# Optimization experiments

Measured on AMD Instinct MI355X. Metric: run time of the kernel, lower is better.

Reference implementation:

```python
import jax, jax.numpy as jnp
import numpy as np

N = 20000        # nodes
E = 320000       # edges
F_IN = 512       # feature_size
H = 512          # hidden_dim (z dim)
OUT = 1024       # output_size


def setup_inputs() -> dict:
    key = jax.random.key(0)
    ks = jax.random.split(key, 24)
    p = lambda k, shape: jax.random.normal(k, shape, jnp.float32) * 0.02
    return {
        "x": jax.random.normal(ks[0], (N, F_IN), jnp.float32),
        "edge_index": jax.random.randint(ks[1], (2, E), 0, N),
        "edge_weight": jax.random.uniform(ks[2], (E,), dtype=jnp.float32),
        "beta": jnp.float32(1.0),
        "y_target": jax.random.uniform(ks[3], (1,), dtype=jnp.float32),
        "eps": jax.random.normal(ks[4], (N, H), jnp.float32),
        # GCNConv weights (in_dim, out_dim) + bias
        "W1": p(ks[5], (F_IN, 1024)), "b1": jnp.zeros((1024,), jnp.float32),
        "W2": p(ks[6], (1024, 512)), "b2": jnp.zeros((512,), jnp.float32),
        "W3": p(ks[7], (512, 256)),  "b3": jnp.zeros((256,), jnp.float32),
        # VAE heads
        "Wmu": p(ks[8], (256, H)),  "bmu": jnp.zeros((H,), jnp.float32),
        "Wlv": p(ks[9], (256, H)),  "blv": jnp.zeros((H,), jnp.float32),
        # decoder MLP: (2H+1) -> (2H+1) -> OUT
        "Wd1": p(ks[10], (2 * H + 1, 2 * H + 1)), "bd1": jnp.zeros((2 * H + 1,), jnp.float32),
        "Wd2": p(ks[11], (2 * H + 1, OUT)),       "bd2": jnp.zeros((OUT,), jnp.float32),
    }


def gcn_conv(x, W, b, src, dst, ew):
    # PyG GCNConv: add self-loops (weight 1), symmetric deg normalization,
    # aggregate normalized neighbor messages of x @ W, then add bias.
    xw = x @ W                                             # [N, out]
    deg = jax.ops.segment_sum(ew, dst, num_segments=N) + 1.0
    dinv = jax.lax.rsqrt(deg)                              # [N]
    norm = dinv[src] * ew * dinv[dst]                      # [E]
    agg = jax.ops.segment_sum(norm[:, None] * xw[src], dst, num_segments=N)
    return agg + (dinv * dinv)[:, None] * xw + b


def l2norm(x):
    n = jnp.sqrt(jnp.sum(x * x, axis=1, keepdims=True))
    return x / jnp.maximum(n, 1e-12)


def reference(x, edge_index, edge_weight, beta, y_target, eps,
              W1, b1, W2, b2, W3, b3, Wmu, bmu, Wlv, blv, Wd1, bd1, Wd2, bd2):
    src, dst = edge_index[0], edge_index[1]
    h = jax.nn.relu(l2norm(gcn_conv(x, W1, b1, src, dst, edge_weight)))
    h = jax.nn.relu(l2norm(gcn_conv(h, W2, b2, src, dst, edge_weight)))
    h = jax.nn.relu(l2norm(gcn_conv(h, W3, b3, src, dst, edge_weight)))
    mu = h @ Wmu + bmu                                     # [N, H]
    logvar = h @ Wlv + blv                                 # [N, H]
    # reparameterize(mu, beta * logvar) with eps ~ 0.01 * N(0,1)
    std = jnp.exp(0.5 * beta * logvar)
    z = mu + (0.01 * eps) * std                            # [N, H]
    out1 = jnp.max(z, axis=0, keepdims=True)               # global max pool [1, H]
    out2 = jnp.mean(z, axis=0, keepdims=True)              # global mean pool [1, H]
    reduce_z = jnp.concatenate([out1, out2, y_target[:, None]], axis=-1)  # [1, 2H+1]
    hdec = jax.nn.relu(reduce_z @ Wd1 + bd1)
    recon_x = jax.nn.sigmoid(hdec @ Wd2 + bd2)             # [1, OUT]
    return (recon_x, mu, logvar)
```

## Files before the change

### kernel.cpp

```cpp
#include <hip/hip_runtime.h>

#define NN 20000
#define EE 320000
#define MPAD 20096
#define MTILES 157
#define DKB 128
#define DCH 9

typedef unsigned short u16;
typedef unsigned int u32;
typedef __attribute__((ext_vector_type(8))) short short8;
typedef __attribute__((ext_vector_type(4))) float f32x4;

__device__ inline float bf16lo(u32 u) { return __uint_as_float(u << 16); }
__device__ inline float bf16hi(u32 u) { return __uint_as_float(u & 0xffff0000u); }
__device__ inline u16 f2b(float f) {
  u32 u = __float_as_uint(f);
  u += 0x7fffu + ((u >> 16) & 1u);
  return (u16)(u >> 16);
}
__device__ inline u32 pack2(float a, float b) {
  return (u32)f2b(a) | ((u32)f2b(b) << 16);
}

__device__ inline void gload16(const void* g, void* l) {
  __builtin_amdgcn_global_load_lds(
      (const __attribute__((address_space(1))) void*)g,
      (__attribute__((address_space(3))) void*)l, 16, 0, 0);
}

__device__ inline int xcd_ord(int wg, int nwg) {
  int q = nwg >> 3, r = nwg & 7;
  int xcd = wg & 7, k = wg >> 3;
  return xcd * q + min(xcd, r) + k;
}

__global__ void k_zeroi(int* __restrict__ p, int n) {
  int i = blockIdx.x * blockDim.x + threadIdx.x;
  if (i < n) p[i] = 0;
}

__global__ void k_f2b2(const float* __restrict__ in, u16* __restrict__ out, int npairs) {
  for (int i = blockIdx.x * blockDim.x + threadIdx.x; i < npairs; i += gridDim.x * blockDim.x) {
    float2 v = *(const float2*)(in + 2 * i);
    ((u32*)out)[i] = pack2(v.x, v.y);
  }
}

__global__ void k_wt_all(const float* __restrict__ W1, const float* __restrict__ W2,
                         const float* __restrict__ W3, const float* __restrict__ Wmu,
                         const float* __restrict__ Wlv,
                         u16* __restrict__ T1, u16* __restrict__ T2,
                         u16* __restrict__ T3, u16* __restrict__ Tmu,
                         u16* __restrict__ Tlv) {
  int b = blockIdx.x;
  const float* W; u16* T; int K, N;
  if (b < 2048)      { W = W1;  T = T1;  K = 512;  N = 1024; }
  else if (b < 4096) { W = W2;  T = T2;  K = 1024; N = 512;  b -= 2048; }
  else if (b < 4608) { W = W3;  T = T3;  K = 512;  N = 256;  b -= 4096; }
  else if (b < 5120) { W = Wmu; T = Tmu; K = 256;  N = 512;  b -= 4608; }
  else               { W = Wlv; T = Tlv; K = 256;  N = 512;  b -= 5120; }
  int kb = K >> 8;
  int n = b / kb;
  int k = (b % kb) * 256 + threadIdx.x;
  T[(size_t)n * K + k] = f2b(W[(size_t)k * N + n]);
}

__global__ void k_count(const int* __restrict__ ei, int* __restrict__ counts) {
  int e = blockIdx.x * blockDim.x + threadIdx.x;
  if (e < EE) atomicAdd(counts + ei[EE + e], 1);
}

__global__ __launch_bounds__(256)
void k_scan(const int* __restrict__ counts, int* __restrict__ rowptr, int* __restrict__ cursor) {
  const int CHUNK = (NN + 255) / 256;
  int t = threadIdx.x;
  int lo = t * CHUNK, hi = min(lo + CHUNK, NN);
  int s = 0;
  for (int i = lo; i < hi; ++i) s += counts[i];
  __shared__ int tsum[256];
  tsum[t] = s;
  __syncthreads();
  if (t == 0) {
    int run = 0;
    for (int i = 0; i < 256; ++i) { int v = tsum[i]; tsum[i] = run; run += v; }
  }
  __syncthreads();
  int run = tsum[t];
  for (int i = lo; i < hi; ++i) {
    rowptr[i] = run;
    cursor[i] = run;
    run += counts[i];
  }
  if (t == 255) rowptr[NN] = EE;
}

__global__ void k_fill(const int* __restrict__ ei, const float* __restrict__ ew,
                       int* __restrict__ cursor, int* __restrict__ colsrc,
                       float* __restrict__ ecw) {
  int e = blockIdx.x * blockDim.x + threadIdx.x;
  if (e < EE) {
    int d = ei[EE + e];
    int pos = atomicAdd(cursor + d, 1);
    colsrc[pos] = ei[e];
    ecw[pos] = ew[e];
  }
}

__global__ void k_degcsr(const int* __restrict__ rowptr, const float* __restrict__ ecw,
                         float* __restrict__ dinv, float* __restrict__ dinv2) {
  int i = blockIdx.x * blockDim.x + threadIdx.x;
  if (i < NN) {
    float s = 0.f;
    for (int e = rowptr[i]; e < rowptr[i + 1]; ++e) s += ecw[e];
    float d = s + 1.0f;
    dinv[i] = rsqrtf(d);
    dinv2[i] = 1.0f / d;
  }
}

template <bool STORE_BF16, bool HAS_BIAS>
__global__ __launch_bounds__(256)
void k_mfma(const u16* __restrict__ A, const u16* __restrict__ BT,
            const float* __restrict__ bias, void* __restrict__ C,
            int M, int K, int N) {
  __shared__ u16 Asm[128 * 32];
  __shared__ u16 Bsm[128 * 32];
  const int tid = threadIdx.x;
  const int ntn = N >> 7;
  int ord = xcd_ord(blockIdx.x, gridDim.x);
  const int m0 = (ord / ntn) * 128;
  const int n0 = (ord % ntn) * 128;
  const int lane = tid & 63;
  const int wave = tid >> 6;
  const int wm = (wave >> 1) * 64;
  const int wn = (wave & 1) * 64;
  const int qm = lane & 15;
  const int quad = lane >> 4;

  f32x4 acc[4][4];
#pragma unroll
  for (int i = 0; i < 4; ++i)
#pragma unroll
    for (int j = 0; j < 4; ++j) acc[i][j] = (f32x4){0.f, 0.f, 0.f, 0.f};

  for (int k0 = 0; k0 < K; k0 += 32) {
#pragma unroll
    for (int h = 0; h < 2; ++h) {
      int c = h * 256 + tid;
      int row = c >> 2, kc = c & 3;
      gload16(A + (size_t)(m0 + row) * K + k0 + kc * 8, Asm + c * 8);
      gload16(BT + (size_t)(n0 + row) * K + k0 + kc * 8, Bsm + c * 8);
    }
    __syncthreads();
    short8 af[4], bfr[4];
#pragma unroll
    for (int i = 0; i < 4; ++i)
      af[i] = *(const short8*)(Asm + (wm + i * 16 + qm) * 32 + quad * 8);
#pragma unroll
    for (int j = 0; j < 4; ++j)
      bfr[j] = *(const short8*)(Bsm + (wn + j * 16 + qm) * 32 + quad * 8);
#pragma unroll
    for (int i = 0; i < 4; ++i)
#pragma unroll
      for (int j = 0; j < 4; ++j)
        acc[i][j] = __builtin_amdgcn_mfma_f32_16x16x32_bf16(af[i], bfr[j], acc[i][j], 0, 0, 0);
    __syncthreads();
  }

#pragma unroll
  for (int i = 0; i < 4; ++i) {
#pragma unroll
    for (int r = 0; r < 4; ++r) {
      int row = m0 + wm + i * 16 + quad * 4 + r;
      if (row >= M) continue;
#pragma unroll
      for (int j = 0; j < 4; ++j) {
        int col = n0 + wn + j * 16 + qm;
        float v = acc[i][j][r];
        if (HAS_BIAS) v += bias[col];
        if (STORE_BF16) ((u16*)C)[(size_t)row * N + col] = f2b(v);
        else ((float*)C)[(size_t)row * N + col] = v;
      }
    }
  }
}

__global__ __launch_bounds__(256, 3)
void k_heads(const u16* __restrict__ A, const u16* __restrict__ BmuT,
             const u16* __restrict__ BlvT, const float* __restrict__ bmu,
             const float* __restrict__ blv, const float* __restrict__ eps,
             const float* __restrict__ beta_p, float* __restrict__ mu_out,
             float* __restrict__ lv_out, float* __restrict__ pmax,
             float* __restrict__ psum) {
  const int K = 256;
  __shared__ float smemf[4352];
  u16* Asm = (u16*)smemf;
  u16* Bmu = (u16*)((char*)smemf + 8192);
  u16* Blv = (u16*)((char*)smemf + 12288);
  float* stmu = smemf;
  float* stlv = smemf + 32 * 68;
  const int tid = threadIdx.x;
  int ord = xcd_ord(blockIdx.x, gridDim.x);
  const int mt = ord >> 3;
  const int m0 = mt * 128;
  const int n0 = (ord & 7) * 64;
  const int lane = tid & 63;
  const int wave = tid >> 6;
  const int wm = (wave >> 1) * 64;
  const int wn = (wave & 1) * 32;
  const int qm = lane & 15;
  const int quad = lane >> 4;

  f32x4 am[4][2], al[4][2];
#pragma unroll
  for (int i = 0; i < 4; ++i)
#pragma unroll
    for (int j = 0; j < 2; ++j) {
      am[i][j] = (f32x4){0.f, 0.f, 0.f, 0.f};
      al[i][j] = (f32x4){0.f, 0.f, 0.f, 0.f};
    }

  for (int k0 = 0; k0 < K; k0 += 32) {
#pragma unroll
    for (int h = 0; h < 2; ++h) {
      int c = h * 256 + tid;
      int row = c >> 2, kc = c & 3;
      gload16(A + (size_t)(m0 + row) * K + k0 + kc * 8, Asm + c * 8);
    }
    {
      int row = tid >> 2, kc = tid & 3;
      gload16(BmuT + (size_t)(n0 + row) * K + k0 + kc * 8, Bmu + tid * 8);
      gload16(BlvT + (size_t)(n0 + row) * K + k0 + kc * 8, Blv + tid * 8);
    }
    __syncthreads();
    short8 af[4], bm[2], bl[2];
#pragma unroll
    for (int i = 0; i < 4; ++i)
      af[i] = *(const short8*)(Asm + (wm + i * 16 + qm) * 32 + quad * 8);
#pragma unroll
    for (int j = 0; j < 2; ++j) {
      bm[j] = *(const short8*)(Bmu + (wn + j * 16 + qm) * 32 + quad * 8);
      bl[j] = *(const short8*)(Blv + (wn + j * 16 + qm) * 32 + quad * 8);
    }
#pragma unroll
    for (int i = 0; i < 4; ++i)
#pragma unroll
      for (int j = 0; j < 2; ++j) {
        am[i][j] = __builtin_amdgcn_mfma_f32_16x16x32_bf16(af[i], bm[j], am[i][j], 0, 0, 0);
        al[i][j] = __builtin_amdgcn_mfma_f32_16x16x32_bf16(af[i], bl[j], al[i][j], 0, 0, 0);
      }
    __syncthreads();
  }

  const float beta = beta_p[0];
  float biasm[2], biasl[2];
#pragma unroll
  for (int j = 0; j < 2; ++j) {
    int col = n0 + wn + j * 16 + qm;
    biasm[j] = bmu[col];
    biasl[j] = blv[col];
  }

  float zmax[8], zsum[8];
#pragma unroll
  for (int q = 0; q < 8; ++q) { zmax[q] = -3.4e38f; zsum[q] = 0.f; }
  const int lrow_r = tid >> 3;
  const int colb = (tid & 7) * 8;

  for (int c = 0; c < 4; ++c) {
    __syncthreads();
    if ((wave >> 1) == (c >> 1)) {
      int ibase = (c & 1) * 2;
#pragma unroll
      for (int ii = 0; ii < 2; ++ii) {
        int i = ibase + ii;
#pragma unroll
        for (int j = 0; j < 2; ++j) {
          int lcol = wn + j * 16 + qm;
#pragma unroll
          for (int r = 0; r < 4; ++r) {
            int lr = ii * 16 + quad * 4 + r;
            stmu[lr * 68 + lcol] = am[i][j][r] + biasm[j];
            stlv[lr * 68 + lcol] = al[i][j][r] + biasl[j];
          }
        }
      }
    }
    __syncthreads();
    int grow = m0 + c * 32 + lrow_r;
    if (grow < NN) {
#pragma unroll
      for (int q4 = 0; q4 < 2; ++q4) {
        int lcol = colb + q4 * 4;
        float4 m4 = *(float4*)(stmu + lrow_r * 68 + lcol);
        float4 l4 = *(float4*)(stlv + lrow_r * 68 + lcol);
        size_t gidx = (size_t)grow * 512 + n0 + lcol;
        float4 e4 = *(const float4*)(eps + gidx);
        *(float4*)(mu_out + gidx) = m4;
        *(float4*)(lv_out + gidx) = l4;
        float z0 = m4.x + 0.01f * e4.x * expf(0.5f * beta * l4.x);
        float z1 = m4.y + 0.01f * e4.y * expf(0.5f * beta * l4.y);
        float z2 = m4.z + 0.01f * e4.z * expf(0.5f * beta * l4.z);
        float z3 = m4.w + 0.01f * e4.w * expf(0.5f * beta * l4.w);
        zmax[q4 * 4 + 0] = fmaxf(zmax[q4 * 4 + 0], z0); zsum[q4 * 4 + 0] += z0;
        zmax[q4 * 4 + 1] = fmaxf(zmax[q4 * 4 + 1], z1); zsum[q4 * 4 + 1] += z1;
        zmax[q4 * 4 + 2] = fmaxf(zmax[q4 * 4 + 2], z2); zsum[q4 * 4 + 2] += z2;
        zmax[q4 * 4 + 3] = fmaxf(zmax[q4 * 4 + 3], z3); zsum[q4 * 4 + 3] += z3;
      }
    }
  }

  __syncthreads();
  float* rbuf = smemf;
#pragma unroll
  for (int q = 0; q < 8; ++q) {
    rbuf[tid * 16 + q] = zmax[q];
    rbuf[tid * 16 + 8 + q] = zsum[q];
  }
  __syncthreads();
  if (tid < 64) {
    int g = tid >> 3, o = tid & 7;
    float m = -3.4e38f, s = 0.f;
    for (int k = 0; k < 32; ++k) {
      int src = (k * 8 + g) * 16;
      m = fmaxf(m, rbuf[src + o]);
      s += rbuf[src + 8 + o];
    }
    pmax[(size_t)mt * 512 + n0 + tid] = m;
    psum[(size_t)mt * 512 + n0 + tid] = s;
  }
}

__global__ void k_zred(const float* __restrict__ pmax, const float* __restrict__ psum,
                       const float* __restrict__ yt, float* __restrict__ rz) {
  int col = threadIdx.x;
  float m = -3.4e38f, s = 0.f;
  for (int c = 0; c < MTILES; ++c) {
    m = fmaxf(m, pmax[(size_t)c * 512 + col]);
    s += psum[(size_t)c * 512 + col];
  }
  rz[col] = m;
  rz[512 + col] = s / (float)NN;
  if (col == 0) rz[1024] = yt[0];
}

template <int NT, bool PRE>
__global__ __launch_bounds__(NT)
void k_gatherv(const int* __restrict__ rowptr, const int* __restrict__ colsrc,
               const float* __restrict__ ecw, const float* __restrict__ dinv,
               const float* __restrict__ dinv2, const u16* __restrict__ xw,
               const float* __restrict__ bias, u16* __restrict__ h) {
  const int O = 4 * NT;
  const int row = blockIdx.x;
  const int tid = threadIdx.x;
  const float dv = dinv[row], dv2 = dinv2[row];
  uint2 u = ((const uint2*)(xw + (size_t)row * O))[tid];
  float a0 = dv2 * bf16lo(u.x), a1 = dv2 * bf16hi(u.x);
  float a2 = dv2 * bf16lo(u.y), a3 = dv2 * bf16hi(u.y);
  if (!PRE) {
    a0 += bias[4 * tid];     a1 += bias[4 * tid + 1];
    a2 += bias[4 * tid + 2]; a3 += bias[4 * tid + 3];
  }
  float c0 = 0.f, c1 = 0.f, c2 = 0.f, c3 = 0.f;

  __shared__ int s_src[NT];
  __shared__ float s_w[NT];
  const int e0 = rowptr[row], e1 = rowptr[row + 1];
  for (int base = e0; base < e1; base += NT) {
    int cnt = min(NT, e1 - base);
    __syncthreads();
    if (tid < cnt) {
      int s = colsrc[base + tid];
      s_src[tid] = s;
      s_w[tid] = dinv[s] * ecw[base + tid] * dv;
    }
    __syncthreads();
    int e = 0;
    for (; e + 2 <= cnt; e += 2) {
      float w0 = s_w[e], w1 = s_w[e + 1];
      uint2 v0 = ((const uint2*)(xw + (size_t)s_src[e] * O))[tid];
      uint2 v1 = ((const uint2*)(xw + (size_t)s_src[e + 1] * O))[tid];
      a0 += w0 * bf16lo(v0.x); a1 += w0 * bf16hi(v0.x);
      a2 += w0 * bf16lo(v0.y); a3 += w0 * bf16hi(v0.y);
      c0 += w1 * bf16lo(v1.x); c1 += w1 * bf16hi(v1.x);
      c2 += w1 * bf16lo(v1.y); c3 += w1 * bf16hi(v1.y);
    }
    if (e < cnt) {
      float w = s_w[e];
      uint2 v = ((const uint2*)(xw + (size_t)s_src[e] * O))[tid];
      a0 += w * bf16lo(v.x); a1 += w * bf16hi(v.x);
      a2 += w * bf16lo(v.y); a3 += w * bf16hi(v.y);
    }
  }
  a0 += c0; a1 += c1; a2 += c2; a3 += c3;

  if (PRE) {
    uint2 o; o.x = pack2(a0, a1); o.y = pack2(a2, a3);
    ((uint2*)(h + (size_t)row * O))[tid] = o;
    return;
  }
  float ss = a0 * a0 + a1 * a1 + a2 * a2 + a3 * a3;
#pragma unroll
  for (int off = 32; off > 0; off >>= 1) ss += __shfl_down(ss, off, 64);
  __shared__ float red[(NT + 63) / 64];
  __shared__ float s_scale;
  if ((tid & 63) == 0) red[tid >> 6] = ss;
  __syncthreads();
  if (tid == 0) {
    float t = 0.f;
#pragma unroll
    for (int i = 0; i < (NT + 63) / 64; ++i) t += red[i];
    s_scale = 1.0f / fmaxf(sqrtf(t), 1e-12f);
  }
  __syncthreads();
  float sc = s_scale;
  uint2 o;
  o.x = pack2(fmaxf(a0 * sc, 0.f), fmaxf(a1 * sc, 0.f));
  o.y = pack2(fmaxf(a2 * sc, 0.f), fmaxf(a3 * sc, 0.f));
  ((uint2*)(h + (size_t)row * O))[tid] = o;
}

__global__ __launch_bounds__(256)
void k_l2relu(const u16* __restrict__ t, u16* __restrict__ h) {
  const int row = blockIdx.x;
  const int tid = threadIdx.x;
  const u32* tr = (const u32*)(t + (size_t)row * 1024);
  u32 u0 = tr[tid], u1 = tr[256 + tid];
  float a0 = bf16lo(u0), a1 = bf16hi(u0), a2 = bf16lo(u1), a3 = bf16hi(u1);
  float ss = a0 * a0 + a1 * a1 + a2 * a2 + a3 * a3;
#pragma unroll
  for (int off = 32; off > 0; off >>= 1) ss += __shfl_down(ss, off, 64);
  __shared__ float red[4];
  __shared__ float s_scale;
  if ((tid & 63) == 0) red[tid >> 6] = ss;
  __syncthreads();
  if (tid == 0) {
    float s = red[0] + red[1] + red[2] + red[3];
    s_scale = 1.0f / fmaxf(sqrtf(s), 1e-12f);
  }
  __syncthreads();
  float sc = s_scale;
  u32* hr = (u32*)(h + (size_t)row * 1024);
  hr[tid]       = pack2(fmaxf(a0 * sc, 0.f), fmaxf(a1 * sc, 0.f));
  hr[256 + tid] = pack2(fmaxf(a2 * sc, 0.f), fmaxf(a3 * sc, 0.f));
}

__global__ __launch_bounds__(256)
void k_dec_partial(const float* __restrict__ v, const float* __restrict__ W,
                   float* __restrict__ partial, int Kdim, int Ndim) {
  int b = blockIdx.x;
  int lo = b * DCH;
  float rv[DCH];
#pragma unroll
  for (int j = 0; j < DCH; ++j) rv[j] = (lo + j < Kdim) ? v[lo + j] : 0.f;
  for (int n = threadIdx.x; n < Ndim; n += 256) {
    float s = 0.f;
#pragma unroll
    for (int j = 0; j < DCH; ++j)
      if (lo + j < Kdim) s += rv[j] * W[(size_t)(lo + j) * Ndim + n];
    partial[(size_t)b * Ndim + n] = s;
  }
}

template <int ACT>
__global__ __launch_bounds__(256)
void k_dec_combine(const float* __restrict__ partial, const float* __restrict__ bias,
                   float* __restrict__ out, int Ndim) {
  int n = blockIdx.x * 256 + threadIdx.x;
  if (n >= Ndim) return;
  float s = bias[n];
  for (int b = 0; b < DKB; ++b) s += partial[(size_t)b * Ndim + n];
  out[n] = (ACT == 0) ? fmaxf(s, 0.f) : 1.0f / (1.0f + expf(-s));
}

extern "C" void kernel_launch(void* const* d_in, const int* in_sizes, int n_in,
                              void* d_out, int out_size, void* d_ws, size_t ws_size,
                              hipStream_t stream) {
  const float* x    = (const float*)d_in[0];
  const int*   ei   = (const int*)d_in[1];
  const float* ew   = (const float*)d_in[2];
  const float* beta = (const float*)d_in[3];
  const float* yt   = (const float*)d_in[4];
  const float* eps  = (const float*)d_in[5];
  const float* W1   = (const float*)d_in[6];  const float* b1  = (const float*)d_in[7];
  const float* W2   = (const float*)d_in[8];  const float* b2  = (const float*)d_in[9];
  const float* W3   = (const float*)d_in[10]; const float* b3  = (const float*)d_in[11];
  const float* Wmu  = (const float*)d_in[12]; const float* bmu = (const float*)d_in[13];
  const float* Wlv  = (const float*)d_in[14]; const float* blv = (const float*)d_in[15];
  const float* Wd1  = (const float*)d_in[16]; const float* bd1 = (const float*)d_in[17];
  const float* Wd2  = (const float*)d_in[18]; const float* bd2 = (const float*)d_in[19];

  char* wsb = (char*)d_ws;
  size_t off = 0;
  auto alloc_f = [&](size_t n) { float* p = (float*)(wsb + off); off += ((n * sizeof(float) + 15) & ~(size_t)15); return p; };
  auto alloc_i = [&](size_t n) { int* p = (int*)(wsb + off); off += ((n * sizeof(int) + 15) & ~(size_t)15); return p; };
  auto alloc_h = [&](size_t n) { u16* p = (u16*)(wsb + off); off += ((n * 2 + 15) & ~(size_t)15); return p; };

  int* counts  = alloc_i(NN);
  int* rowptr  = alloc_i(NN + 1);
  int* cursor  = alloc_i(NN);
  int* colsrc  = alloc_i(EE);
  float* ecw   = alloc_f(EE);
  float* dinv  = alloc_f(NN);
  float* din2  = alloc_f(NN);
  float* pmax  = alloc_f((size_t)MTILES * 512);
  float* psum  = alloc_f((size_t)MTILES * 512);
  float* rz    = alloc_f(1028);
  float* hdec  = alloc_f(1028);
  float* part1 = alloc_f((size_t)DKB * 1025);
  float* part2 = alloc_f((size_t)DKB * 1024);
  u16* W1T  = alloc_h(1024 * 512);
  u16* W2T  = alloc_h(512 * 1024);
  u16* W3T  = alloc_h(256 * 512);
  u16* WmuT = alloc_h(512 * 256);
  u16* WlvT = alloc_h(512 * 256);
  u16* xb   = alloc_h((size_t)MPAD * 512);
  u16* aggx = alloc_h((size_t)MPAD * 512);
  u16* bufT = alloc_h((size_t)MPAD * 1024);
  u16* bufH = alloc_h((size_t)MPAD * 1024);
  u16* h2   = alloc_h((size_t)MPAD * 512);
  u16* h3   = xb;
  u16* z2   = bufT;
  u16* z3   = bufH;

  float* out_f  = (float*)d_out;
  float* mu_out = out_f + 1024;
  float* lv_out = out_f + 1024 + (size_t)NN * 512;

  const int MT = MTILES;

  k_f2b2<<<4096, 256, 0, stream>>>(x, xb, NN * 512 / 2);
  k_wt_all<<<5632, 256, 0, stream>>>(W1, W2, W3, Wmu, Wlv, W1T, W2T, W3T, WmuT, WlvT);

  k_zeroi<<<(NN + 255) / 256, 256, 0, stream>>>(counts, NN);
  k_count<<<(EE + 255) / 256, 256, 0, stream>>>(ei, counts);
  k_scan<<<1, 256, 0, stream>>>(counts, rowptr, cursor);
  k_fill<<<(EE + 255) / 256, 256, 0, stream>>>(ei, ew, cursor, colsrc, ecw);
  k_degcsr<<<(NN + 255) / 256, 256, 0, stream>>>(rowptr, ecw, dinv, din2);

  k_gatherv<128, true><<<NN, 128, 0, stream>>>(rowptr, colsrc, ecw, dinv, din2, xb, nullptr, aggx);
  k_mfma<true, true><<<MT * 8, 256, 0, stream>>>(aggx, W1T, b1, bufT, NN, 512, 1024);
  k_l2relu<<<NN, 256, 0, stream>>>(bufT, bufH);

  k_mfma<true, false><<<MT * 4, 256, 0, stream>>>(bufH, W2T, nullptr, z2, NN, 1024, 512);
  k_gatherv<128, false><<<NN, 128, 0, stream>>>(rowptr, colsrc, ecw, dinv, din2, z2, b2, h2);

  k_mfma<true, false><<<MT * 2, 256, 0, stream>>>(h2, W3T, nullptr, z3, NN, 512, 256);
  k_gatherv<64, false><<<NN, 64, 0, stream>>>(rowptr, colsrc, ecw, dinv, din2, z3, b3, h3);

  k_heads<<<MT * 8, 256, 0, stream>>>(h3, WmuT, WlvT, bmu, blv, eps, beta,
                                      mu_out, lv_out, pmax, psum);
  k_zred<<<1, 512, 0, stream>>>(pmax, psum, yt, rz);

  k_dec_partial<<<DKB, 256, 0, stream>>>(rz, Wd1, part1, 1025, 1025);
  k_dec_combine<0><<<5, 256, 0, stream>>>(part1, bd1, hdec, 1025);
  k_dec_partial<<<DKB, 256, 0, stream>>>(hdec, Wd2, part2, 1025, 1024);
  k_dec_combine<1><<<4, 256, 0, stream>>>(part2, bd2, out_f, 1024);
}
```

Before: 645.2 us.

## Double-buffer LDS tiles in MFMA GEMM to overlap loads with compute

```diff
diff --git a/kernel.cpp b/kernel.cpp
--- a/kernel.cpp
+++ b/kernel.cpp
@@ -124,8 +124,8 @@
 void k_mfma(const u16* __restrict__ A, const u16* __restrict__ BT,
             const float* __restrict__ bias, void* __restrict__ C,
             int M, int K, int N) {
-  __shared__ u16 Asm[128 * 32];
-  __shared__ u16 Bsm[128 * 32];
+  __shared__ u16 Asm[2][128 * 32];
+  __shared__ u16 Bsm[2][128 * 32];
   const int tid = threadIdx.x;
   const int ntn = N >> 7;
   int ord = xcd_ord(blockIdx.x, gridDim.x);
@@ -144,28 +144,44 @@
 #pragma unroll
     for (int j = 0; j < 4; ++j) acc[i][j] = (f32x4){0.f, 0.f, 0.f, 0.f};
 
-  for (int k0 = 0; k0 < K; k0 += 32) {
-#pragma unroll
-    for (int h = 0; h < 2; ++h) {
-      int c = h * 256 + tid;
-      int row = c >> 2, kc = c & 3;
-      gload16(A + (size_t)(m0 + row) * K + k0 + kc * 8, Asm + c * 8);
-      gload16(BT + (size_t)(n0 + row) * K + k0 + kc * 8, Bsm + c * 8);
-    }
-    __syncthreads();
+  const int row_s = tid >> 2, kc_s = (tid & 3) * 8;
+
+#pragma unroll
+  for (int h = 0; h < 2; ++h) {
+    int row = h * 64 + row_s;
+    gload16(A + (size_t)(m0 + row) * K + kc_s, Asm[0] + row * 32 + kc_s);
+    gload16(BT + (size_t)(n0 + row) * K + kc_s, Bsm[0] + row * 32 + kc_s);
+  }
+  __syncthreads();
+
+  const int nk = K >> 5;
+  int cur = 0;
+  for (int t = 0; t < nk; ++t) {
+    if (t + 1 < nk) {
+      int k1 = (t + 1) * 32;
+#pragma unroll
+      for (int h = 0; h < 2; ++h) {
+        int row = h * 64 + row_s;
+        gload16(A + (size_t)(m0 + row) * K + k1 + kc_s, Asm[cur ^ 1] + row * 32 + kc_s);
+        gload16(BT + (size_t)(n0 + row) * K + k1 + kc_s, Bsm[cur ^ 1] + row * 32 + kc_s);
+      }
+    }
     short8 af[4], bfr[4];
 #pragma unroll
     for (int i = 0; i < 4; ++i)
-      af[i] = *(const short8*)(Asm + (wm + i * 16 + qm) * 32 + quad * 8);
+      af[i] = *(const short8*)(Asm[cur] + (wm + i * 16 + qm) * 32 + quad * 8);
 #pragma unroll
     for (int j = 0; j < 4; ++j)
-      bfr[j] = *(const short8*)(Bsm + (wn + j * 16 + qm) * 32 + quad * 8);
+      bfr[j] = *(const short8*)(Bsm[cur] + (wn + j * 16 + qm) * 32 + quad * 8);
 #pragma unroll
     for (int i = 0; i < 4; ++i)
 #pragma unroll
       for (int j = 0; j < 4; ++j)
         acc[i][j] = __builtin_amdgcn_mfma_f32_16x16x32_bf16(af[i], bfr[j], acc[i][j], 0, 0, 0);
-    __syncthreads();
+    if (t + 1 < nk) {
+      __syncthreads();
+      cur ^= 1;
+    }
   }
 
 #pragma unroll
```

Result: no change. 641.1 us (-0.6%).
